# Optimization experiments

Hardware: AMD Instinct MI355X
Metric: run time of the kernel (lower is better)

The kernel has to match this reference:

```python
import jax, jax.numpy as jnp
import numpy as np

DIM = 2048
H = 16        # num query heads
KVH = 4       # num kv heads
HD = DIM // H # head_dim = 128
RD = 64       # rope_dims (< head_dim -> partial rope)
BASE = 10000.0
SCALE = HD ** -0.5
EPS_RMS = 1e-6
EPS_NORM = 1e-12


def _rms_norm(x):
    return x * jax.lax.rsqrt(jnp.mean(x * x, axis=-1, keepdims=True) + EPS_RMS)


def _rope_cache(T):
    inv_freq = 1.0 / (BASE ** (jnp.arange(0, RD, 2, dtype=jnp.float32) / RD))  # [RD/2]
    t = jnp.arange(T, dtype=jnp.float32)
    freqs = t[:, None] * inv_freq[None, :]  # [T, RD/2]
    return jnp.cos(freqs)[None, None], jnp.sin(freqs)[None, None]  # [1,1,T,RD/2]


def _apply_rope(x, cos, sin):
    # x: [B, H, T, HD]; rotate first RD dims, pass through the rest
    x_rope, x_pass = x[..., :RD], x[..., RD:]
    half = RD // 2
    x1, x2 = x_rope[..., :half], x_rope[..., half:]
    x_rot = jnp.concatenate([x1 * cos - x2 * sin, x2 * cos + x1 * sin], axis=-1)
    return jnp.concatenate([x_rot, x_pass], axis=-1)


def setup_inputs() -> dict:
    key = jax.random.key(0)
    ks = jax.random.split(key, 6)
    x = jax.random.normal(ks[0], (4, 2048, DIM), dtype=jnp.float32)
    Wq = jax.random.normal(ks[1], (DIM, DIM), dtype=jnp.float32) * 0.02
    Wk = jax.random.normal(ks[2], (KVH * HD, DIM), dtype=jnp.float32) * 0.02
    Wv = jax.random.normal(ks[3], (KVH * HD, DIM), dtype=jnp.float32) * 0.02
    Wproj = jax.random.normal(ks[4], (DIM, DIM), dtype=jnp.float32) * 0.02
    q_gain = jnp.ones((H,), dtype=jnp.float32)
    return {"x": x, "Wq": Wq, "Wk": Wk, "Wv": Wv, "Wproj": Wproj, "q_gain": q_gain}


def reference(x, Wq, Wk, Wv, Wproj, q_gain):
    B, T, _ = x.shape
    # projections (nn.Linear: x @ W.T)  ->  [B, heads, T, HD]
    q = (x @ Wq.T).reshape(B, T, H, HD).transpose(0, 2, 1, 3)
    k = (x @ Wk.T).reshape(B, T, KVH, HD).transpose(0, 2, 1, 3)
    v = (x @ Wv.T).reshape(B, T, KVH, HD).transpose(0, 2, 1, 3)

    cos, sin = _rope_cache(T)
    q = _apply_rope(_rms_norm(q), cos, sin) * q_gain[None, :, None, None]
    k = _apply_rope(_rms_norm(k), cos, sin)

    # GQA: expand kv heads (kv head i serves query heads i*rep .. i*rep+rep-1)
    rep = H // KVH
    k = jnp.repeat(k, rep, axis=1)      # [B, H, T, HD]
    v_attn = jnp.repeat(v, rep, axis=1)  # [B, H, T, HD]

    # causal SDPA
    scores = jnp.einsum("bhqd,bhkd->bhqk", q, k) * SCALE
    causal = jnp.tril(jnp.ones((T, T), dtype=bool))
    scores = jnp.where(causal[None, None], scores, jnp.finfo(scores.dtype).min)
    attn = jax.nn.softmax(scores, axis=-1)
    y = jnp.einsum("bhqk,bhkd->bhqd", attn, v_attn)

    # xsa postproc: remove component of y along unit value direction
    vn = v_attn / jnp.maximum(
        jnp.linalg.norm(v_attn, axis=-1, keepdims=True), EPS_NORM)
    y = y - jnp.sum(y * vn, axis=-1, keepdims=True) * vn

    y = y.transpose(0, 2, 1, 3).reshape(B, T, DIM)
    return y @ Wproj.T
```

## Files before the change

kernel.cpp:

```cpp
#include <hip/hip_runtime.h>
#include <cstdint>
#include <cstddef>

typedef __bf16 bf16_t;
typedef __bf16 bf16x4 __attribute__((ext_vector_type(4)));
typedef __bf16 bf16x8 __attribute__((ext_vector_type(8)));
typedef float f32x4 __attribute__((ext_vector_type(4)));

#define B_ 4
#define T_ 2048
#define DIM_ 2048
#define H_ 16
#define KVH_ 4
#define HD_ 128
#define QKV_ 3072
#define QSCALE (0.08838834764831845f * 1.4426950408889634f)

__device__ __forceinline__ void gload16(const bf16_t* g, bf16_t* l) {
  __builtin_amdgcn_global_load_lds(
      (const __attribute__((address_space(1))) unsigned int*)g,
      (__attribute__((address_space(3))) unsigned int*)l, 16, 0, 0);
}

__global__ __launch_bounds__(256) void cvt_all(const float4* __restrict__ x,
                                               const float4* __restrict__ wq,
                                               const float4* __restrict__ wk,
                                               const float4* __restrict__ wv,
                                               const float4* __restrict__ wp,
                                               bf16x4* __restrict__ xb,
                                               bf16x4* __restrict__ wqkvb,
                                               bf16x4* __restrict__ wpb) {
  int i = blockIdx.x * 256 + threadIdx.x;
  const float4* s;
  bf16x4* dst;
  int off;
  if (i < 4194304) { s = x; dst = xb; off = i; }
  else if (i < 5242880) { s = wq; dst = wqkvb; off = i - 4194304; }
  else if (i < 5505024) { s = wk; dst = wqkvb + 1048576; off = i - 5242880; }
  else if (i < 5767168) { s = wv; dst = wqkvb + 1310720; off = i - 5505024; }
  else { s = wp; dst = wpb; off = i - 5767168; }
  float4 v = s[off];
  bf16x4 o = {(__bf16)v.x, (__bf16)v.y, (__bf16)v.z, (__bf16)v.w};
  dst[off] = o;
}

__global__ __launch_bounds__(256) void gemm_bt(const bf16_t* __restrict__ A,
                                               const bf16_t* __restrict__ B,
                                               void* __restrict__ Cp,
                                               int M, int N, int K, int out_bf16) {
  __shared__ bf16_t As[128 * 32];
  __shared__ bf16_t Bs[128 * 32];
  const int tid = threadIdx.x;
  const int w = tid >> 6, lane = tid & 63;
  const int m_lane = lane & 15, quad = lane >> 4;
  const int wr = w >> 1, wc = w & 1;
  const int rowBase = blockIdx.y * 128, colBase = blockIdx.x * 128;

  f32x4 acc[4][4];
#pragma unroll
  for (int i = 0; i < 4; ++i)
#pragma unroll
    for (int j = 0; j < 4; ++j) acc[i][j] = (f32x4){0.f, 0.f, 0.f, 0.f};

  const int nk = K >> 5;
  for (int kk = 0; kk < nk; ++kk) {
    const int k0 = kk << 5;
#pragma unroll
    for (int i2 = 0; i2 < 2; ++i2) {
      int idx = i2 * 256 + tid;
      int row = idx >> 2, kc = idx & 3;
      gload16(A + (size_t)(rowBase + row) * K + k0 + kc * 8, &As[idx * 8]);
      gload16(B + (size_t)(colBase + row) * K + k0 + kc * 8, &Bs[idx * 8]);
    }
    __syncthreads();
    bf16x8 a[4], bb[4];
#pragma unroll
    for (int i = 0; i < 4; ++i)
      a[i] = *(const bf16x8*)&As[(wr * 64 + i * 16 + m_lane) * 32 + quad * 8];
#pragma unroll
    for (int j = 0; j < 4; ++j)
      bb[j] = *(const bf16x8*)&Bs[(wc * 64 + j * 16 + m_lane) * 32 + quad * 8];
#pragma unroll
    for (int i = 0; i < 4; ++i)
#pragma unroll
      for (int j = 0; j < 4; ++j)
        acc[i][j] = __builtin_amdgcn_mfma_f32_16x16x32_bf16(a[i], bb[j], acc[i][j], 0, 0, 0);
    __syncthreads();
  }

  if (out_bf16) {
    bf16_t* C = (bf16_t*)Cp;
#pragma unroll
    for (int i = 0; i < 4; ++i)
#pragma unroll
      for (int j = 0; j < 4; ++j)
#pragma unroll
        for (int r = 0; r < 4; ++r) {
          int row = rowBase + wr * 64 + i * 16 + quad * 4 + r;
          int col = colBase + wc * 64 + j * 16 + m_lane;
          C[(size_t)row * N + col] = (bf16_t)acc[i][j][r];
        }
  } else {
    float* C = (float*)Cp;
#pragma unroll
    for (int i = 0; i < 4; ++i)
#pragma unroll
      for (int j = 0; j < 4; ++j)
#pragma unroll
        for (int r = 0; r < 4; ++r) {
          int row = rowBase + wr * 64 + i * 16 + quad * 4 + r;
          int col = colBase + wc * 64 + j * 16 + m_lane;
          C[(size_t)row * N + col] = acc[i][j][r];
        }
  }
}

__global__ __launch_bounds__(256) void gemm_qkv(const bf16_t* __restrict__ A,
                                                const bf16_t* __restrict__ Bw,
                                                bf16_t* __restrict__ qkv,
                                                bf16_t* __restrict__ vt,
                                                const float* __restrict__ gain) {
  __shared__ bf16_t As[128 * 32];
  __shared__ bf16_t Bs[128 * 32];
  __shared__ float ssbuf[2][128];
  const int tid = threadIdx.x;
  const int w = tid >> 6, lane = tid & 63;
  const int m = lane & 15, quad = lane >> 4;
  const int wr = w >> 1, wc = w & 1;
  const int rowBase = blockIdx.y * 128, colBase = blockIdx.x * 128;

  f32x4 acc[4][4];
#pragma unroll
  for (int i = 0; i < 4; ++i)
#pragma unroll
    for (int j = 0; j < 4; ++j) acc[i][j] = (f32x4){0.f, 0.f, 0.f, 0.f};

  for (int kk = 0; kk < 64; ++kk) {
    const int k0 = kk << 5;
#pragma unroll
    for (int i2 = 0; i2 < 2; ++i2) {
      int idx = i2 * 256 + tid;
      int row = idx >> 2, kc = idx & 3;
      gload16(A + (size_t)(rowBase + row) * 2048 + k0 + kc * 8, &As[idx * 8]);
      gload16(Bw + (size_t)(colBase + row) * 2048 + k0 + kc * 8, &Bs[idx * 8]);
    }
    __syncthreads();
    bf16x8 a[4], bb[4];
#pragma unroll
    for (int i = 0; i < 4; ++i)
      a[i] = *(const bf16x8*)&As[(wr * 64 + i * 16 + m) * 32 + quad * 8];
#pragma unroll
    for (int j = 0; j < 4; ++j)
      bb[j] = *(const bf16x8*)&Bs[(wc * 64 + j * 16 + m) * 32 + quad * 8];
#pragma unroll
    for (int i = 0; i < 4; ++i)
#pragma unroll
      for (int j = 0; j < 4; ++j)
        acc[i][j] = __builtin_amdgcn_mfma_f32_16x16x32_bf16(a[i], bb[j], acc[i][j], 0, 0, 0);
    __syncthreads();
  }

  const int bx = blockIdx.x;
  if (bx < 20) {
    const float g = (bx < 16) ? gain[bx] * QSCALE : 1.0f;
#pragma unroll
    for (int i = 0; i < 4; ++i) {
      float ssp[4];
#pragma unroll
      for (int r = 0; r < 4; ++r) {
        float s = 0.f;
#pragma unroll
        for (int j = 0; j < 4; ++j) s += acc[i][j][r] * acc[i][j][r];
#pragma unroll
        for (int off = 1; off <= 8; off <<= 1) s += __shfl_xor(s, off);
        ssp[r] = s;
      }
      if (m == 0) {
#pragma unroll
        for (int r = 0; r < 4; ++r) ssbuf[wc][wr * 64 + i * 16 + quad * 4 + r] = ssp[r];
      }
    }
    __syncthreads();
    const float if0 = exp2f(-(float)m * 0.4152410118609203f);
    const float if1 = exp2f(-(float)(16 + m) * 0.4152410118609203f);
#pragma unroll
    for (int i = 0; i < 4; ++i) {
#pragma unroll
      for (int r = 0; r < 4; ++r) {
        const int ridx = wr * 64 + i * 16 + quad * 4 + r;
        const int row = rowBase + ridx;
        const float rn = rsqrtf((ssbuf[0][ridx] + ssbuf[1][ridx]) * (1.f / 128.f) + 1e-6f);
        float v0 = acc[i][0][r] * rn, v1 = acc[i][1][r] * rn;
        float v2 = acc[i][2][r] * rn, v3 = acc[i][3][r] * rn;
        float o0 = v0, o1 = v1, o2 = v2, o3 = v3;
        if (wc == 0) {
          const float t = (float)(row & (T_ - 1));
          const float a0 = t * if0, a1 = t * if1;
          const float c0 = cosf(a0), s0 = sinf(a0);
          const float c1 = cosf(a1), s1 = sinf(a1);
          o0 = v0 * c0 - v2 * s0;
          o1 = v1 * c1 - v3 * s1;
          o2 = v2 * c0 + v0 * s0;
          o3 = v3 * c1 + v1 * s1;
        }
        bf16_t* out = qkv + (size_t)row * QKV_ + colBase + wc * 64 + m;
        out[0]  = (bf16_t)(o0 * g);
        out[16] = (bf16_t)(o1 * g);
        out[32] = (bf16_t)(o2 * g);
        out[48] = (bf16_t)(o3 * g);
      }
    }
  } else {
    const int kvh = bx - 20;
#pragma unroll
    for (int i = 0; i < 4; ++i)
#pragma unroll
      for (int j = 0; j < 4; ++j) {
        const int row0 = rowBase + wr * 64 + i * 16 + quad * 4;
        const int d = wc * 64 + j * 16 + m;
        bf16x4 pv;
#pragma unroll
        for (int r = 0; r < 4; ++r) {
          pv[r] = (bf16_t)acc[i][j][r];
          qkv[(size_t)(row0 + r) * QKV_ + colBase + d] = pv[r];
        }
        const int b = row0 >> 11, t0 = row0 & (T_ - 1);
        *(bf16x4*)(vt + ((size_t)(b * KVH_ + kvh) * HD_ + d) * T_ + t0) = pv;
      }
  }
}

__global__ __launch_bounds__(256) void attn_kernel(const bf16_t* __restrict__ qkv,
                                                   const bf16_t* __restrict__ vt,
                                                   bf16_t* __restrict__ y) {
  __shared__ __align__(16) bf16_t Ks[2][32 * 128];
  __shared__ __align__(16) bf16_t Vs[2][128 * 32];
  __shared__ __align__(16) bf16_t Ps[4][32 * 40];

  const int tid = threadIdx.x;
  const int w = tid >> 6, lane = tid & 63;
  const int m = lane & 15, q = lane >> 4;
  const int h = blockIdx.y, b = blockIdx.z, kvh = h >> 2;

  const bf16_t* qptr = qkv + (size_t)(b * T_) * QKV_ + h * HD_;
  const bf16_t* kptr = qkv + (size_t)(b * T_) * QKV_ + DIM_ + kvh * HD_;
  const bf16_t* vptr = qkv + (size_t)(b * T_) * QKV_ + DIM_ + KVH_ * HD_ + kvh * HD_;
  const bf16_t* vtptr = vt + (size_t)(b * KVH_ + kvh) * HD_ * T_;

  const int kKey0 = tid >> 4, kC0 = tid & 15;
  const int kKey1 = (256 + tid) >> 4, kC1 = tid & 15;
  const int vD0 = tid >> 2, vC0 = tid & 3;
  const int vD1 = (256 + tid) >> 2, vC1 = tid & 3;
  const int vS0 = (vD0 ^ (vD0 >> 2)) & 3, vS1 = (vD1 ^ (vD1 >> 2)) & 3;

  int koff[2][4], voff[8], poff[2];
#pragma unroll
  for (int kf = 0; kf < 2; ++kf)
#pragma unroll
    for (int c = 0; c < 4; ++c)
      koff[kf][c] = (kf * 16 + m) * 128 + (((c * 4 + q) ^ m) & 15) * 8;
#pragma unroll
  for (int f = 0; f < 8; ++f) {
    const int d = f * 16 + m;
    voff[f] = d * 32 + ((q ^ ((d ^ (d >> 2)) & 3)) & 3) * 8;
  }
#pragma unroll
  for (int qf = 0; qf < 2; ++qf) poff[qf] = (qf * 16 + m) * 40 + q * 8;

#pragma unroll 1
  for (int ti = 0; ti < 2; ++ti) {
    const int qb = ((ti == 0) ? (15 - (int)blockIdx.x) : (int)blockIdx.x) * 128;
    const int qbw = qb + w * 32;
    const int nk = (qb >> 5) + 4;

    bf16x8 aq[2][4];
#pragma unroll
    for (int qf = 0; qf < 2; ++qf)
#pragma unroll
      for (int c = 0; c < 4; ++c)
        aq[qf][c] = *(const bf16x8*)(qptr + (size_t)(qbw + qf * 16 + m) * QKV_ + c * 32 + q * 8);

    f32x4 o[2][8];
#pragma unroll
    for (int qf = 0; qf < 2; ++qf)
#pragma unroll
      for (int f = 0; f < 8; ++f) o[qf][f] = (f32x4){0.f, 0.f, 0.f, 0.f};
    float l_r[2] = {0.f, 0.f};

    {
      gload16(kptr + (size_t)kKey0 * QKV_ + ((kC0 ^ kKey0) & 15) * 8, &Ks[0][tid * 8]);
      gload16(kptr + (size_t)kKey1 * QKV_ + ((kC1 ^ kKey1) & 15) * 8, &Ks[0][(256 + tid) * 8]);
      gload16(vtptr + (size_t)vD0 * T_ + (vC0 ^ vS0) * 8, &Vs[0][tid * 8]);
      gload16(vtptr + (size_t)vD1 * T_ + (vC1 ^ vS1) * 8, &Vs[0][(256 + tid) * 8]);
    }

#pragma unroll 1
    for (int it = 0; it < nk; ++it) {
      const int kb = it << 5;
      __syncthreads();

      if (it + 1 < nk) {
        const int kb2 = kb + 32;
        bf16_t* Kb = Ks[(it + 1) & 1];
        bf16_t* Vb = Vs[(it + 1) & 1];
        gload16(kptr + (size_t)(kb2 + kKey0) * QKV_ + ((kC0 ^ kKey0) & 15) * 8, &Kb[tid * 8]);
        gload16(kptr + (size_t)(kb2 + kKey1) * QKV_ + ((kC1 ^ kKey1) & 15) * 8, &Kb[(256 + tid) * 8]);
        gload16(vtptr + (size_t)vD0 * T_ + kb2 + (vC0 ^ vS0) * 8, &Vb[tid * 8]);
        gload16(vtptr + (size_t)vD1 * T_ + kb2 + (vC1 ^ vS1) * 8, &Vb[(256 + tid) * 8]);
      }

      if (kb > qbw + 31) continue;
      const bf16_t* Kb = Ks[it & 1];
      const bf16_t* Vb = Vs[it & 1];

      f32x4 S[2][2];
#pragma unroll
      for (int qf = 0; qf < 2; ++qf)
#pragma unroll
        for (int kf = 0; kf < 2; ++kf) S[qf][kf] = (f32x4){0.f, 0.f, 0.f, 0.f};
#pragma unroll
      for (int kf = 0; kf < 2; ++kf)
#pragma unroll
        for (int c = 0; c < 4; ++c) {
          bf16x8 ak = *(const bf16x8*)&Kb[koff[kf][c]];
          S[0][kf] = __builtin_amdgcn_mfma_f32_16x16x32_bf16(ak, aq[0][c], S[0][kf], 0, 0, 0);
          S[1][kf] = __builtin_amdgcn_mfma_f32_16x16x32_bf16(ak, aq[1][c], S[1][kf], 0, 0, 0);
        }

      const bool needmask = (kb + 31) > qbw;
#pragma unroll
      for (int qf = 0; qf < 2; ++qf) {
        const int qrow = qbw + qf * 16 + m;
        if (needmask) {
#pragma unroll
          for (int kf = 0; kf < 2; ++kf)
#pragma unroll
            for (int r = 0; r < 4; ++r) {
              int key = kb + kf * 16 + q * 4 + r;
              if (key > qrow) S[qf][kf][r] = -1e30f;
            }
        }
        float rs = 0.f;
#pragma unroll
        for (int kf = 0; kf < 2; ++kf)
#pragma unroll
          for (int r = 0; r < 4; ++r) {
            float p = exp2f(S[qf][kf][r]);
            S[qf][kf][r] = p;
            rs += p;
          }
        rs += __shfl_xor(rs, 16);
        rs += __shfl_xor(rs, 32);
        l_r[qf] += rs;
#pragma unroll
        for (int kf = 0; kf < 2; ++kf) {
          bf16x4 pk = {(__bf16)S[qf][kf][0], (__bf16)S[qf][kf][1],
                       (__bf16)S[qf][kf][2], (__bf16)S[qf][kf][3]};
          *(bf16x4*)&Ps[w][(qf * 16 + m) * 40 + kf * 16 + q * 4] = pk;
        }
      }
      asm volatile("s_waitcnt lgkmcnt(0)" ::: "memory");

      bf16x8 Pb[2];
#pragma unroll
      for (int qf = 0; qf < 2; ++qf)
        Pb[qf] = *(const bf16x8*)&Ps[w][poff[qf]];
#pragma unroll
      for (int f = 0; f < 8; ++f) {
        bf16x8 av = *(const bf16x8*)&Vb[voff[f]];
        o[0][f] = __builtin_amdgcn_mfma_f32_16x16x32_bf16(av, Pb[0], o[0][f], 0, 0, 0);
        o[1][f] = __builtin_amdgcn_mfma_f32_16x16x32_bf16(av, Pb[1], o[1][f], 0, 0, 0);
      }
    }

#pragma unroll
    for (int qf = 0; qf < 2; ++qf) {
      const int trow = qbw + qf * 16 + m;
      const float linv = 1.f / l_r[qf];
      bf16x4 vv[8];
      float n2 = 0.f, dp = 0.f;
#pragma unroll
      for (int f = 0; f < 8; ++f) {
        vv[f] = *(const bf16x4*)(vptr + (size_t)trow * QKV_ + f * 16 + q * 4);
#pragma unroll
        for (int r = 0; r < 4; ++r) {
          float v = (float)vv[f][r];
          n2 += v * v;
          dp += o[qf][f][r] * linv * v;
        }
      }
      n2 += __shfl_xor(n2, 16); n2 += __shfl_xor(n2, 32);
      dp += __shfl_xor(dp, 16); dp += __shfl_xor(dp, 32);
      float d = fmaxf(sqrtf(n2), 1e-12f);
      float coef = dp / (d * d);
#pragma unroll
      for (int f = 0; f < 8; ++f) {
        bf16x4 yo;
#pragma unroll
        for (int r = 0; r < 4; ++r)
          yo[r] = (bf16_t)(o[qf][f][r] * linv - coef * (float)vv[f][r]);
        *(bf16x4*)(y + (size_t)(b * T_ + trow) * DIM_ + h * HD_ + f * 16 + q * 4) = yo;
      }
    }
    __syncthreads();
  }
}

extern "C" void kernel_launch(void* const* d_in, const int* in_sizes, int n_in,
                              void* d_out, int out_size, void* d_ws, size_t ws_size,
                              hipStream_t stream) {
  const float* x = (const float*)d_in[0];
  const float* Wq = (const float*)d_in[1];
  const float* Wk = (const float*)d_in[2];
  const float* Wv = (const float*)d_in[3];
  const float* Wp = (const float*)d_in[4];
  const float* qg = (const float*)d_in[5];

  bf16_t* xbf = (bf16_t*)d_ws;
  bf16_t* wqkv = xbf + (size_t)8192 * 2048;
  bf16_t* wproj = wqkv + (size_t)3072 * 2048;
  bf16_t* qkv = wproj + (size_t)2048 * 2048;
  bf16_t* vt = qkv + (size_t)8192 * 3072;
  bf16_t* ybf = xbf;

  cvt_all<<<26624, 256, 0, stream>>>((const float4*)x, (const float4*)Wq,
                                     (const float4*)Wk, (const float4*)Wv,
                                     (const float4*)Wp, (bf16x4*)xbf,
                                     (bf16x4*)wqkv, (bf16x4*)wproj);
  gemm_qkv<<<dim3(24, 64), 256, 0, stream>>>(xbf, wqkv, qkv, vt, qg);
  attn_kernel<<<dim3(8, 16, 4), 256, 0, stream>>>(qkv, vt, ybf);
  gemm_bt<<<dim3(16, 64), 256, 0, stream>>>(ybf, wproj, d_out, 8192, 2048, 2048, 0);
}
```

Baseline: 551.8 us.

## Double-buffer LDS tiles in GEMM kernels to overlap global loads with MFMA

Both the generic bt GEMM and the fused QKV GEMM now keep two LDS buffers for the A and B tiles. The next k-tile is prefetched with global_load_lds while MFMAs run on the current one, and only one barrier remains per iteration instead of two. The goal is to hide global-memory latency behind compute. It doubles LDS use per block, which may lower occupancy, and the RoPE temporaries are renamed to avoid clashing with the new loader variables.

```diff
diff --git a/kernel.cpp b/kernel.cpp
--- a/kernel.cpp
+++ b/kernel.cpp
@@ -48,44 +48,54 @@
                                                const bf16_t* __restrict__ B,
                                                void* __restrict__ Cp,
                                                int M, int N, int K, int out_bf16) {
-  __shared__ bf16_t As[128 * 32];
-  __shared__ bf16_t Bs[128 * 32];
+  __shared__ bf16_t As[2][128 * 32];
+  __shared__ bf16_t Bs[2][128 * 32];
   const int tid = threadIdx.x;
   const int w = tid >> 6, lane = tid & 63;
   const int m_lane = lane & 15, quad = lane >> 4;
   const int wr = w >> 1, wc = w & 1;
   const int rowBase = blockIdx.y * 128, colBase = blockIdx.x * 128;
 
+  const int r0 = tid >> 2, c0 = tid & 3;
+  const int r1 = (256 + tid) >> 2, c1 = tid & 3;
+
   f32x4 acc[4][4];
 #pragma unroll
   for (int i = 0; i < 4; ++i)
 #pragma unroll
     for (int j = 0; j < 4; ++j) acc[i][j] = (f32x4){0.f, 0.f, 0.f, 0.f};
+
+  gload16(A + (size_t)(rowBase + r0) * K + c0 * 8, &As[0][tid * 8]);
+  gload16(B + (size_t)(colBase + r0) * K + c0 * 8, &Bs[0][tid * 8]);
+  gload16(A + (size_t)(rowBase + r1) * K + c1 * 8, &As[0][(256 + tid) * 8]);
+  gload16(B + (size_t)(colBase + r1) * K + c1 * 8, &Bs[0][(256 + tid) * 8]);
 
   const int nk = K >> 5;
   for (int kk = 0; kk < nk; ++kk) {
-    const int k0 = kk << 5;
-#pragma unroll
-    for (int i2 = 0; i2 < 2; ++i2) {
-      int idx = i2 * 256 + tid;
-      int row = idx >> 2, kc = idx & 3;
-      gload16(A + (size_t)(rowBase + row) * K + k0 + kc * 8, &As[idx * 8]);
-      gload16(B + (size_t)(colBase + row) * K + k0 + kc * 8, &Bs[idx * 8]);
-    }
     __syncthreads();
+    if (kk + 1 < nk) {
+      const int k0 = (kk + 1) << 5;
+      bf16_t* Ad = As[(kk + 1) & 1];
+      bf16_t* Bd = Bs[(kk + 1) & 1];
+      gload16(A + (size_t)(rowBase + r0) * K + k0 + c0 * 8, &Ad[tid * 8]);
+      gload16(B + (size_t)(colBase + r0) * K + k0 + c0 * 8, &Bd[tid * 8]);
+      gload16(A + (size_t)(rowBase + r1) * K + k0 + c1 * 8, &Ad[(256 + tid) * 8]);
+      gload16(B + (size_t)(colBase + r1) * K + k0 + c1 * 8, &Bd[(256 + tid) * 8]);
+    }
+    const bf16_t* Ab = As[kk & 1];
+    const bf16_t* Bb = Bs[kk & 1];
     bf16x8 a[4], bb[4];
 #pragma unroll
     for (int i = 0; i < 4; ++i)
-      a[i] = *(const bf16x8*)&As[(wr * 64 + i * 16 + m_lane) * 32 + quad * 8];
+      a[i] = *(const bf16x8*)&Ab[(wr * 64 + i * 16 + m_lane) * 32 + quad * 8];
 #pragma unroll
     for (int j = 0; j < 4; ++j)
-      bb[j] = *(const bf16x8*)&Bs[(wc * 64 + j * 16 + m_lane) * 32 + quad * 8];
+      bb[j] = *(const bf16x8*)&Bb[(wc * 64 + j * 16 + m_lane) * 32 + quad * 8];
 #pragma unroll
     for (int i = 0; i < 4; ++i)
 #pragma unroll
       for (int j = 0; j < 4; ++j)
         acc[i][j] = __builtin_amdgcn_mfma_f32_16x16x32_bf16(a[i], bb[j], acc[i][j], 0, 0, 0);
-    __syncthreads();
   }
 
   if (out_bf16) {
@@ -120,8 +130,8 @@
                                                 bf16_t* __restrict__ qkv,
                                                 bf16_t* __restrict__ vt,
                                                 const float* __restrict__ gain) {
-  __shared__ bf16_t As[128 * 32];
-  __shared__ bf16_t Bs[128 * 32];
+  __shared__ bf16_t As[2][128 * 32];
+  __shared__ bf16_t Bs[2][128 * 32];
   __shared__ float ssbuf[2][128];
   const int tid = threadIdx.x;
   const int w = tid >> 6, lane = tid & 63;
@@ -129,35 +139,45 @@
   const int wr = w >> 1, wc = w & 1;
   const int rowBase = blockIdx.y * 128, colBase = blockIdx.x * 128;
 
+  const int r0 = tid >> 2, c0 = tid & 3;
+  const int r1 = (256 + tid) >> 2, c1 = tid & 3;
+
   f32x4 acc[4][4];
 #pragma unroll
   for (int i = 0; i < 4; ++i)
 #pragma unroll
     for (int j = 0; j < 4; ++j) acc[i][j] = (f32x4){0.f, 0.f, 0.f, 0.f};
 
+  gload16(A + (size_t)(rowBase + r0) * 2048 + c0 * 8, &As[0][tid * 8]);
+  gload16(Bw + (size_t)(colBase + r0) * 2048 + c0 * 8, &Bs[0][tid * 8]);
+  gload16(A + (size_t)(rowBase + r1) * 2048 + c1 * 8, &As[0][(256 + tid) * 8]);
+  gload16(Bw + (size_t)(colBase + r1) * 2048 + c1 * 8, &Bs[0][(256 + tid) * 8]);
+
   for (int kk = 0; kk < 64; ++kk) {
-    const int k0 = kk << 5;
-#pragma unroll
-    for (int i2 = 0; i2 < 2; ++i2) {
-      int idx = i2 * 256 + tid;
-      int row = idx >> 2, kc = idx & 3;
-      gload16(A + (size_t)(rowBase + row) * 2048 + k0 + kc * 8, &As[idx * 8]);
-      gload16(Bw + (size_t)(colBase + row) * 2048 + k0 + kc * 8, &Bs[idx * 8]);
-    }
     __syncthreads();
+    if (kk + 1 < 64) {
+      const int k0 = (kk + 1) << 5;
+      bf16_t* Ad = As[(kk + 1) & 1];
+      bf16_t* Bd = Bs[(kk + 1) & 1];
+      gload16(A + (size_t)(rowBase + r0) * 2048 + k0 + c0 * 8, &Ad[tid * 8]);
+      gload16(Bw + (size_t)(colBase + r0) * 2048 + k0 + c0 * 8, &Bd[tid * 8]);
+      gload16(A + (size_t)(rowBase + r1) * 2048 + k0 + c1 * 8, &Ad[(256 + tid) * 8]);
+      gload16(Bw + (size_t)(colBase + r1) * 2048 + k0 + c1 * 8, &Bd[(256 + tid) * 8]);
+    }
+    const bf16_t* Ab = As[kk & 1];
+    const bf16_t* Bb = Bs[kk & 1];
     bf16x8 a[4], bb[4];
 #pragma unroll
     for (int i = 0; i < 4; ++i)
-      a[i] = *(const bf16x8*)&As[(wr * 64 + i * 16 + m) * 32 + quad * 8];
+      a[i] = *(const bf16x8*)&Ab[(wr * 64 + i * 16 + m) * 32 + quad * 8];
 #pragma unroll
     for (int j = 0; j < 4; ++j)
-      bb[j] = *(const bf16x8*)&Bs[(wc * 64 + j * 16 + m) * 32 + quad * 8];
+      bb[j] = *(const bf16x8*)&Bb[(wc * 64 + j * 16 + m) * 32 + quad * 8];
 #pragma unroll
     for (int i = 0; i < 4; ++i)
 #pragma unroll
       for (int j = 0; j < 4; ++j)
         acc[i][j] = __builtin_amdgcn_mfma_f32_16x16x32_bf16(a[i], bb[j], acc[i][j], 0, 0, 0);
-    __syncthreads();
   }
 
   const int bx = blockIdx.x;
@@ -196,12 +216,12 @@
         if (wc == 0) {
           const float t = (float)(row & (T_ - 1));
           const float a0 = t * if0, a1 = t * if1;
-          const float c0 = cosf(a0), s0 = sinf(a0);
-          const float c1 = cosf(a1), s1 = sinf(a1);
-          o0 = v0 * c0 - v2 * s0;
-          o1 = v1 * c1 - v3 * s1;
-          o2 = v2 * c0 + v0 * s0;
-          o3 = v3 * c1 + v1 * s1;
+          const float c0_ = cosf(a0), s0_ = sinf(a0);
+          const float c1_ = cosf(a1), s1_ = sinf(a1);
+          o0 = v0 * c0_ - v2 * s0_;
+          o1 = v1 * c1_ - v3 * s1_;
+          o2 = v2 * c0_ + v0 * s0_;
+          o3 = v3 * c1_ + v1 * s1_;
         }
         bf16_t* out = qkv + (size_t)row * QKV_ + colBase + wc * 64 + m;
         out[0]  = (bf16_t)(o0 * g);
```

Result: slower. 571.8 us (+3.6%).

## Rewrite output projection GEMM with 256x256 tiles, double-buffered LDS and swizzle

Applied to the files above, without the earlier changes.

Rebuilds the final projection GEMM as a 512-thread kernel that computes 256x256 output tiles with K steps of 64. Tiles are double-buffered in LDS and loaded with global_load_lds, using an XOR swizzle to avoid bank conflicts. Barriers, waitcnt and setprio are interleaved so the next tile's loads overlap the MFMA work. This aims to raise arithmetic intensity and hide load latency, at the cost of 128 KB of LDS, more registers and only 256 blocks. The rope variable renames are cosmetic.

```diff
diff --git a/kernel.cpp b/kernel.cpp
--- a/kernel.cpp
+++ b/kernel.cpp
@@ -44,72 +44,143 @@
   dst[off] = o;
 }
 
-__global__ __launch_bounds__(256) void gemm_bt(const bf16_t* __restrict__ A,
-                                               const bf16_t* __restrict__ B,
-                                               void* __restrict__ Cp,
-                                               int M, int N, int K, int out_bf16) {
-  __shared__ bf16_t As[128 * 32];
-  __shared__ bf16_t Bs[128 * 32];
+#define STAGE2(gsrc, ldst)                                   \
+  do {                                                       \
+    gload16((gsrc), (ldst) + tid * 8);                       \
+    gload16((gsrc) + (size_t)128 * K, (ldst) + 4096 + tid * 8); \
+  } while (0)
+
+__global__ __launch_bounds__(512, 2) void gemm_bt(const bf16_t* __restrict__ A,
+                                                  const bf16_t* __restrict__ B,
+                                                  void* __restrict__ Cp,
+                                                  int M, int N, int K, int out_bf16) {
+  __shared__ __align__(16) bf16_t Ab[2 * 16384];
+  __shared__ __align__(16) bf16_t Bb[2 * 16384];
   const int tid = threadIdx.x;
   const int w = tid >> 6, lane = tid & 63;
-  const int m_lane = lane & 15, quad = lane >> 4;
-  const int wr = w >> 1, wc = w & 1;
-  const int rowBase = blockIdx.y * 128, colBase = blockIdx.x * 128;
-
-  f32x4 acc[4][4];
-#pragma unroll
-  for (int i = 0; i < 4; ++i)
+  const int m16 = lane & 15, q4 = lane >> 4;
+  const int wr = w >> 2, wc = w & 3;
+  const int rowBase = blockIdx.y * 256, colBase = blockIdx.x * 256;
+
+  const int srow = tid >> 2, skc = tid & 3;
+  const bf16_t* srcA = A + (size_t)(rowBase + srow) * K + (skc ^ (srow & 3)) * 8;
+  const bf16_t* srcB = B + (size_t)(colBase + srow) * K + (skc ^ (srow & 3)) * 8;
+
+  const int cs = (q4 ^ m16) & 3;
+  const int aoff = wr * 4096 + m16 * 32 + cs * 8;
+  const int boff = wc * 2048 + m16 * 32 + cs * 8;
+
+  f32x4 acc[8][4];
+#pragma unroll
+  for (int i = 0; i < 8; ++i)
 #pragma unroll
     for (int j = 0; j < 4; ++j) acc[i][j] = (f32x4){0.f, 0.f, 0.f, 0.f};
 
-  const int nk = K >> 5;
-  for (int kk = 0; kk < nk; ++kk) {
-    const int k0 = kk << 5;
-#pragma unroll
-    for (int i2 = 0; i2 < 2; ++i2) {
-      int idx = i2 * 256 + tid;
-      int row = idx >> 2, kc = idx & 3;
-      gload16(A + (size_t)(rowBase + row) * K + k0 + kc * 8, &As[idx * 8]);
-      gload16(B + (size_t)(colBase + row) * K + k0 + kc * 8, &Bs[idx * 8]);
-    }
-    __syncthreads();
-    bf16x8 a[4], bb[4];
-#pragma unroll
-    for (int i = 0; i < 4; ++i)
-      a[i] = *(const bf16x8*)&As[(wr * 64 + i * 16 + m_lane) * 32 + quad * 8];
-#pragma unroll
-    for (int j = 0; j < 4; ++j)
-      bb[j] = *(const bf16x8*)&Bs[(wc * 64 + j * 16 + m_lane) * 32 + quad * 8];
-#pragma unroll
-    for (int i = 0; i < 4; ++i)
-#pragma unroll
-      for (int j = 0; j < 4; ++j)
-        acc[i][j] = __builtin_amdgcn_mfma_f32_16x16x32_bf16(a[i], bb[j], acc[i][j], 0, 0, 0);
-    __syncthreads();
+  const int nt = K >> 6;
+  STAGE2(srcA, Ab);
+  STAGE2(srcB, Bb);
+  STAGE2(srcA + 32, Ab + 8192);
+  STAGE2(srcB + 32, Bb + 8192);
+  asm volatile("s_waitcnt vmcnt(4)" ::: "memory");
+  __builtin_amdgcn_s_barrier();
+
+#pragma unroll 1
+  for (int t = 0; t < nt; ++t) {
+    const int cb = (t & 1) << 14, nb = cb ^ 16384;
+    const int pk = ((t + 1 < nt) ? t + 1 : t) << 6;
+    const bf16_t* Ac = Ab + cb + aoff;
+    const bf16_t* Bc = Bb + cb + boff;
+    bf16x8 a[4], b[4];
+
+    STAGE2(srcA + pk, Ab + nb);
+#pragma unroll
+    for (int i = 0; i < 4; ++i) a[i] = *(const bf16x8*)(Ac + i * 512);
+#pragma unroll
+    for (int j = 0; j < 4; ++j) b[j] = *(const bf16x8*)(Bc + j * 512);
+    __builtin_amdgcn_s_barrier();
+    asm volatile("s_waitcnt lgkmcnt(0)" ::: "memory");
+    __builtin_amdgcn_sched_barrier(0);
+    __builtin_amdgcn_s_setprio(1);
+#pragma unroll
+    for (int i = 0; i < 4; ++i)
+#pragma unroll
+      for (int j = 0; j < 4; ++j)
+        acc[i][j] = __builtin_amdgcn_mfma_f32_16x16x32_bf16(a[i], b[j], acc[i][j], 0, 0, 0);
+    __builtin_amdgcn_s_setprio(0);
+    __builtin_amdgcn_s_barrier();
+
+    STAGE2(srcB + pk, Bb + nb);
+#pragma unroll
+    for (int i = 0; i < 4; ++i) a[i] = *(const bf16x8*)(Ac + (4 + i) * 512);
+    __builtin_amdgcn_s_barrier();
+    asm volatile("s_waitcnt lgkmcnt(0)" ::: "memory");
+    __builtin_amdgcn_sched_barrier(0);
+    __builtin_amdgcn_s_setprio(1);
+#pragma unroll
+    for (int i = 0; i < 4; ++i)
+#pragma unroll
+      for (int j = 0; j < 4; ++j)
+        acc[4 + i][j] = __builtin_amdgcn_mfma_f32_16x16x32_bf16(a[i], b[j], acc[4 + i][j], 0, 0, 0);
+    __builtin_amdgcn_s_setprio(0);
+    asm volatile("s_waitcnt vmcnt(4)" ::: "memory");
+    __builtin_amdgcn_s_barrier();
+
+    STAGE2(srcA + pk + 32, Ab + nb + 8192);
+#pragma unroll
+    for (int i = 0; i < 4; ++i) a[i] = *(const bf16x8*)(Ac + 8192 + i * 512);
+#pragma unroll
+    for (int j = 0; j < 4; ++j) b[j] = *(const bf16x8*)(Bc + 8192 + j * 512);
+    __builtin_amdgcn_s_barrier();
+    asm volatile("s_waitcnt lgkmcnt(0)" ::: "memory");
+    __builtin_amdgcn_sched_barrier(0);
+    __builtin_amdgcn_s_setprio(1);
+#pragma unroll
+    for (int i = 0; i < 4; ++i)
+#pragma unroll
+      for (int j = 0; j < 4; ++j)
+        acc[i][j] = __builtin_amdgcn_mfma_f32_16x16x32_bf16(a[i], b[j], acc[i][j], 0, 0, 0);
+    __builtin_amdgcn_s_setprio(0);
+    __builtin_amdgcn_s_barrier();
+
+    STAGE2(srcB + pk + 32, Bb + nb + 8192);
+#pragma unroll
+    for (int i = 0; i < 4; ++i) a[i] = *(const bf16x8*)(Ac + 8192 + (4 + i) * 512);
+    __builtin_amdgcn_s_barrier();
+    asm volatile("s_waitcnt lgkmcnt(0)" ::: "memory");
+    __builtin_amdgcn_sched_barrier(0);
+    __builtin_amdgcn_s_setprio(1);
+#pragma unroll
+    for (int i = 0; i < 4; ++i)
+#pragma unroll
+      for (int j = 0; j < 4; ++j)
+        acc[4 + i][j] = __builtin_amdgcn_mfma_f32_16x16x32_bf16(a[i], b[j], acc[4 + i][j], 0, 0, 0);
+    __builtin_amdgcn_s_setprio(0);
+    asm volatile("s_waitcnt vmcnt(4)" ::: "memory");
+    __builtin_amdgcn_s_barrier();
   }
 
   if (out_bf16) {
     bf16_t* C = (bf16_t*)Cp;
 #pragma unroll
-    for (int i = 0; i < 4; ++i)
+    for (int i = 0; i < 8; ++i)
 #pragma unroll
       for (int j = 0; j < 4; ++j)
 #pragma unroll
         for (int r = 0; r < 4; ++r) {
-          int row = rowBase + wr * 64 + i * 16 + quad * 4 + r;
-          int col = colBase + wc * 64 + j * 16 + m_lane;
+          int row = rowBase + wr * 128 + i * 16 + q4 * 4 + r;
+          int col = colBase + wc * 64 + j * 16 + m16;
           C[(size_t)row * N + col] = (bf16_t)acc[i][j][r];
         }
   } else {
     float* C = (float*)Cp;
 #pragma unroll
-    for (int i = 0; i < 4; ++i)
+    for (int i = 0; i < 8; ++i)
 #pragma unroll
       for (int j = 0; j < 4; ++j)
 #pragma unroll
         for (int r = 0; r < 4; ++r) {
-          int row = rowBase + wr * 64 + i * 16 + quad * 4 + r;
-          int col = colBase + wc * 64 + j * 16 + m_lane;
+          int row = rowBase + wr * 128 + i * 16 + q4 * 4 + r;
+          int col = colBase + wc * 64 + j * 16 + m16;
           C[(size_t)row * N + col] = acc[i][j][r];
         }
   }
@@ -196,12 +267,12 @@
         if (wc == 0) {
           const float t = (float)(row & (T_ - 1));
           const float a0 = t * if0, a1 = t * if1;
-          const float c0 = cosf(a0), s0 = sinf(a0);
-          const float c1 = cosf(a1), s1 = sinf(a1);
-          o0 = v0 * c0 - v2 * s0;
-          o1 = v1 * c1 - v3 * s1;
-          o2 = v2 * c0 + v0 * s0;
-          o3 = v3 * c1 + v1 * s1;
+          const float c0_ = cosf(a0), s0_ = sinf(a0);
+          const float c1_ = cosf(a1), s1_ = sinf(a1);
+          o0 = v0 * c0_ - v2 * s0_;
+          o1 = v1 * c1_ - v3 * s1_;
+          o2 = v2 * c0_ + v0 * s0_;
+          o3 = v3 * c1_ + v1 * s1_;
         }
         bf16_t* out = qkv + (size_t)row * QKV_ + colBase + wc * 64 + m;
         out[0]  = (bf16_t)(o0 * g);
@@ -429,5 +500,5 @@
                                      (bf16x4*)wqkv, (bf16x4*)wproj);
   gemm_qkv<<<dim3(24, 64), 256, 0, stream>>>(xbf, wqkv, qkv, vt, qg);
   attn_kernel<<<dim3(8, 16, 4), 256, 0, stream>>>(qkv, vt, ybf);
-  gemm_bt<<<dim3(16, 64), 256, 0, stream>>>(ybf, wproj, d_out, 8192, 2048, 2048, 0);
+  gemm_bt<<<dim3(8, 32), 512, 0, stream>>>(ybf, wproj, d_out, 8192, 2048, 2048, 0);
 }
```

Result: no change. 546.9 us (-0.9%).
